# Performance work log

Measured on AMD Instinct MI355X. Metric: run time of the kernel, lower is better.

## Reference

```python
import jax, jax.numpy as jnp
import numpy as np

B, S, D, H = 4, 2048, 1024, 16
DK = D // H


def setup_inputs() -> dict:
    key = jax.random.key(0)
    ks = jax.random.split(key, 5)
    scale = 1.0 / np.sqrt(D)
    return {
        "embeddings": jax.random.normal(ks[0], (B, S, D), dtype=jnp.float32),
        "W_q": jax.random.normal(ks[1], (D, D), dtype=jnp.float32) * scale,
        "W_k": jax.random.normal(ks[2], (D, D), dtype=jnp.float32) * scale,
        "W_v": jax.random.normal(ks[3], (D, D), dtype=jnp.float32) * scale,
        "W_o": jax.random.normal(ks[4], (D, D), dtype=jnp.float32) * scale,
    }


def reference(embeddings, W_q, W_k, W_v, W_o):
    # torch Linear: y = x @ W.T  (weights stored [out, in])
    def proj(x, W):
        # [B,S,D] -> [B,H,S,DK]
        y = jnp.einsum("bsd,ed->bse", x, W)
        return y.reshape(B, S, H, DK).transpose(0, 2, 1, 3)

    Q = proj(embeddings, W_q)
    K = proj(embeddings, W_k)
    V = proj(embeddings, W_v)

    scores = jnp.einsum("bhqd,bhkd->bhqk", Q, K) / jnp.sqrt(jnp.float32(DK))
    p_attn = jax.nn.softmax(scores, axis=-1)  # dropout p=0.0 -> identity
    x = jnp.einsum("bhqk,bhkd->bhqd", p_attn, V)
    x = x.transpose(0, 2, 1, 3).reshape(B, S, D)
    return jnp.einsum("bsd,ed->bse", x, W_o)
```

## Files before the change

### kernel.cpp

```cpp
#include <hip/hip_runtime.h>
#include <hip/hip_bf16.h>

#define BB 4
#define SS 2048
#define DD 1024
#define HH 16
#define MM (BB * SS)

typedef __attribute__((ext_vector_type(8))) short bf16x8;
typedef __attribute__((ext_vector_type(4))) float f32x4;

__device__ __forceinline__ unsigned short f2bf(float f) {
  union { float f; unsigned u; } v; v.f = f;
  unsigned r = v.u + 0x7fffu + ((v.u >> 16) & 1u);
  return (unsigned short)(r >> 16);
}

__device__ __forceinline__ void gl2lds16(const void* g, void* l) {
  __builtin_amdgcn_global_load_lds(
      (const __attribute__((address_space(1))) unsigned int*)g,
      (__attribute__((address_space(3))) unsigned int*)l, 16, 0, 0);
}

__global__ __launch_bounds__(256)
void convall(const float* __restrict__ X, const float* __restrict__ a,
             const float* __restrict__ b, const float* __restrict__ c,
             const float* __restrict__ d, unsigned short* __restrict__ wall,
             unsigned short* __restrict__ xb) {
  int y = blockIdx.y;
  const float* s; unsigned short* o; float scl = 1.0f;
  if (y < 4) {
    const float* srcs[4] = {a, b, c, d};
    s = srcs[y]; o = wall + (size_t)y * 1048576;
    if (y == 0) scl = 0.180336880f;
  } else {
    s = X + (size_t)(y - 4) * 1048576; o = xb + (size_t)(y - 4) * 1048576;
  }
  int i = (blockIdx.x * 256 + threadIdx.x) * 4;
  float4 v = *(const float4*)(s + i);
  ushort4 h4;
  h4.x = f2bf(v.x * scl); h4.y = f2bf(v.y * scl);
  h4.z = f2bf(v.z * scl); h4.w = f2bf(v.w * scl);
  *(ushort4*)(o + i) = h4;
}

__global__ __launch_bounds__(512, 2)
void gemm256(const unsigned short* __restrict__ A16, const unsigned short* __restrict__ Bp,
             unsigned short* __restrict__ Qo, unsigned short* __restrict__ Ko,
             unsigned short* __restrict__ Vt) {
  extern __shared__ unsigned short L[];
  const int Lid = blockIdx.x;
  const int wg = (Lid & 7) * 48 + (Lid >> 3);
  const int mx = wg & 31, ny = wg >> 5;
  const int m0 = mx * 256, n0g = ny * 256;

  const int tid = threadIdx.x, lane = tid & 63, wv = tid >> 6;
  const int wave_m = wv >> 2, wave_n = wv & 3;
  const int row_in = lane & 15, quad = lane >> 4;

  const int srow = lane >> 3;
  const int sc = ((lane & 7) ^ (lane >> 3)) * 8;
  const unsigned short* gA0 = A16 + (size_t)(m0 + srow) * DD + sc;
  const unsigned short* gB0 = Bp + (size_t)(n0g + srow) * DD + sc;

  const int aoff = (wave_m * 128 + row_in) * 64;
  const int boff = (wave_n * 64 + row_in) * 64;
  const int swz0 = ((quad) ^ (row_in & 7)) * 8;
  const int swz1 = ((4 + quad) ^ (row_in & 7)) * 8;

  f32x4 acc[8][4] = {};

#define SA(a, par, kbv)                                                         \
  do {                                                                          \
    const int ld_ = (par) * 16384 + (a) * 8192 + (wv * 16) * 64;                \
    gl2lds16(gA0 + (size_t)((a) * 128 + wv * 16 + 0) * DD + (kbv), L + ld_);    \
    gl2lds16(gA0 + (size_t)((a) * 128 + wv * 16 + 8) * DD + (kbv), L + ld_ + 512); \
  } while (0)
#define SBf(par, kbv)                                                           \
  do {                                                                          \
    const int ld_ = 32768 + (par) * 16384 + (wv * 32) * 64;                     \
    gl2lds16(gB0 + (size_t)(wv * 32 + 0) * DD + (kbv), L + ld_);                \
    gl2lds16(gB0 + (size_t)(wv * 32 + 8) * DD + (kbv), L + ld_ + 512);          \
    gl2lds16(gB0 + (size_t)(wv * 32 + 16) * DD + (kbv), L + ld_ + 1024);        \
    gl2lds16(gB0 + (size_t)(wv * 32 + 24) * DD + (kbv), L + ld_ + 1536);        \
  } while (0)
#define LDA(par, mh, swzv)                                                      \
  do {                                                                          \
    _Pragma("unroll") for (int f = 0; f < 4; ++f)                               \
        af[f] = *(const bf16x8*)(L + (par) * 16384 + aoff + ((mh) * 64 + f * 16) * 64 + (swzv)); \
  } while (0)
#define LDB(par, swzv)                                                          \
  do {                                                                          \
    _Pragma("unroll") for (int nf = 0; nf < 4; ++nf)                            \
        bk[nf] = *(const bf16x8*)(L + 32768 + (par) * 16384 + boff + nf * 1024 + (swzv)); \
  } while (0)
#define MFMA16(mh)                                                              \
  do {                                                                          \
    __builtin_amdgcn_s_setprio(1);                                              \
    _Pragma("unroll") for (int f = 0; f < 4; ++f)                               \
        _Pragma("unroll") for (int nf = 0; nf < 4; ++nf)                        \
            acc[(mh) * 4 + f][nf] = __builtin_amdgcn_mfma_f32_16x16x32_bf16(    \
                af[f], bk[nf], acc[(mh) * 4 + f][nf], 0, 0, 0);                 \
    __builtin_amdgcn_s_setprio(0);                                              \
  } while (0)
#define PBAR()                                 \
  do {                                         \
    asm volatile("" ::: "memory");             \
    __builtin_amdgcn_s_barrier();              \
    asm volatile("" ::: "memory");             \
  } while (0)
#define PWAIT(n) asm volatile("s_waitcnt vmcnt(" #n ")" ::: "memory")

  SA(0, 0, 0);
  SBf(0, 0);
  SA(1, 0, 0);
  SA(0, 1, 64);

  for (int i = 0; i < 8; ++i) {
    const int kb1 = (2 * i + 1) * 64;
    const int t2 = 2 * i + 2, t3 = 2 * i + 3;
    const int kb2 = (t2 < 16 ? t2 : 15) * 64;
    const int kb3 = (t3 < 16 ? t3 : 15) * 64;
    bf16x8 af[4], bk[4];
    PWAIT(4); PBAR();
    LDB(0, swz0); LDA(0, 0, swz0);
    SBf(1, kb1);
    MFMA16(0);
    PWAIT(6); PBAR();
    LDA(0, 1, swz0);
    SA(1, 1, kb1);
    MFMA16(1);
    PBAR();
    LDB(0, swz1); LDA(0, 0, swz1);
    MFMA16(0);
    PBAR();
    LDA(0, 1, swz1);
    SA(0, 0, kb2);
    MFMA16(1);
    PWAIT(4); PBAR();
    LDB(1, swz0); LDA(1, 0, swz0);
    SBf(0, kb2);
    MFMA16(0);
    PWAIT(6); PBAR();
    LDA(1, 1, swz0);
    SA(1, 0, kb2);
    MFMA16(1);
    PBAR();
    LDB(1, swz1); LDA(1, 0, swz1);
    MFMA16(0);
    PBAR();
    LDA(1, 1, swz1);
    SA(0, 1, kb3);
    MFMA16(1);
  }
  asm volatile("s_waitcnt vmcnt(0)" ::: "memory");
#undef SA
#undef SBf
#undef LDA
#undef LDB
#undef MFMA16
#undef PBAR
#undef PWAIT

  const int seg = n0g >> 10;
  if (seg < 2) {
    unsigned short* Cout = (seg == 0) ? Qo : Ko;
    const int n0 = n0g & 1023;
#pragma unroll
    for (int mh = 0; mh < 2; ++mh)
#pragma unroll
      for (int f = 0; f < 4; ++f)
#pragma unroll
        for (int nf = 0; nf < 4; ++nf)
#pragma unroll
          for (int r2 = 0; r2 < 4; ++r2)
            Cout[(size_t)(m0 + wave_m * 128 + mh * 64 + f * 16 + quad * 4 + r2) * DD +
                 n0 + wave_n * 64 + nf * 16 + row_in] = f2bf(acc[mh * 4 + f][nf][r2]);
  } else {
    const int b = m0 >> 11;
    const int ktb = ((m0 & 2047) >> 6) + wave_m * 2;
    const int h = ((n0g - 2048) >> 6) + wave_n;
#pragma unroll
    for (int mh = 0; mh < 2; ++mh) {
      const int kt = ktb + mh;
#pragma unroll
      for (int nf = 0; nf < 4; ++nf) {
        unsigned short v[16];
#pragma unroll
        for (int j = 0; j < 16; ++j)
          v[j] = f2bf(acc[mh * 4 + (j & 3)][nf][j >> 2]);
        unsigned short* dst = Vt + ((size_t)((b * 16 + h) * 64 + nf * 16 + row_in)) * SS +
                              kt * 64 + quad * 16;
        *(uint4*)dst = *(const uint4*)v;
        *(uint4*)(dst + 8) = *(const uint4*)(v + 8);
      }
    }
  }
}

__global__ __launch_bounds__(256)
void gemm_o(const unsigned short* __restrict__ A16, const unsigned short* __restrict__ Bp,
            float* __restrict__ Cout) {
  __shared__ unsigned short As[2 * 4096];
  __shared__ unsigned short Bs[2 * 4096];
  const int m0 = blockIdx.x * 128, n0g = blockIdx.y * 128;
  const int tid = threadIdx.x, lane = tid & 63, wave = tid >> 6;
  const int wm = (wave & 1) * 64, wn = (wave >> 1) * 64;
  const int row_in = lane & 15, quad = lane >> 4;

  f32x4 acc[4][4] = {};

  const int r = wave * 32 + (lane >> 2);
  const unsigned short* gB = Bp + (size_t)(n0g + r) * DD + (lane & 3) * 8;
  const unsigned short* gA = A16 + (size_t)(m0 + r) * DD + (lane & 3) * 8;

  gl2lds16(gB, Bs + (wave * 32) * 32);
  gl2lds16(gB + (size_t)16 * DD, Bs + (wave * 32 + 16) * 32);
  gl2lds16(gA, As + (wave * 32) * 32);
  gl2lds16(gA + (size_t)16 * DD, As + (wave * 32 + 16) * 32);

  int cur = 0;
  for (int kb = 0; kb < DD; kb += 32) {
    __syncthreads();
    if (kb + 32 < DD) {
      const int nx = (cur ^ 1) * 4096;
      gl2lds16(gB + kb + 32, Bs + nx + (wave * 32) * 32);
      gl2lds16(gB + kb + 32 + (size_t)16 * DD, Bs + nx + (wave * 32 + 16) * 32);
      gl2lds16(gA + kb + 32, As + nx + (wave * 32) * 32);
      gl2lds16(gA + kb + 32 + (size_t)16 * DD, As + nx + (wave * 32 + 16) * 32);
    }
    const int cb = cur * 4096;
    bf16x8 af[4], bfr[4];
#pragma unroll
    for (int i = 0; i < 4; ++i)
      af[i] = *(const bf16x8*)(As + cb + (wm + i * 16 + row_in) * 32 + quad * 8);
#pragma unroll
    for (int j = 0; j < 4; ++j)
      bfr[j] = *(const bf16x8*)(Bs + cb + (wn + j * 16 + row_in) * 32 + quad * 8);
    __builtin_amdgcn_s_setprio(1);
#pragma unroll
    for (int i = 0; i < 4; ++i)
#pragma unroll
      for (int j = 0; j < 4; ++j)
        acc[i][j] = __builtin_amdgcn_mfma_f32_16x16x32_bf16(af[i], bfr[j], acc[i][j], 0, 0, 0);
    __builtin_amdgcn_s_setprio(0);
    cur ^= 1;
  }
  __syncthreads();

#pragma unroll
  for (int i = 0; i < 4; ++i)
#pragma unroll
    for (int j = 0; j < 4; ++j)
#pragma unroll
      for (int r2 = 0; r2 < 4; ++r2)
        Cout[(size_t)(m0 + wm + i * 16 + quad * 4 + r2) * DD + n0g + wn + j * 16 + row_in] =
            acc[i][j][r2];
}

__global__ __launch_bounds__(256, 4)
void attn_kernel(const unsigned short* __restrict__ Q, const unsigned short* __restrict__ K,
                 const unsigned short* __restrict__ Vt_g, unsigned short* __restrict__ AO) {
  __shared__ unsigned short Ks[64 * 72];
  __shared__ unsigned short Vs[64 * 72];
  __shared__ unsigned short Ps[128 * 72];
  const int L = (blockIdx.y << 4) + blockIdx.x;
  const int jj = L >> 3;
  const int qt = jj & 15;
  const int bh = (L & 7) + ((jj >> 4) << 3);
  const int b = bh >> 4, h = bh & 15;
  const int tid = threadIdx.x, lane = tid & 63, w = tid >> 6;
  const int row_in = lane & 15, quad = lane >> 4;
  const size_t qbase = ((size_t)(b * SS + qt * 128)) * DD + h * 64;

  bf16x8 aq[2][2];
#pragma unroll
  for (int m = 0; m < 2; ++m) {
    const unsigned short* qp = Q + qbase + (size_t)(w * 32 + m * 16 + row_in) * DD;
    aq[m][0] = *(const bf16x8*)(qp + quad * 8);
    aq[m][1] = *(const bf16x8*)(qp + 32 + quad * 8);
  }
  f32x4 oacc[2][4] = {};
  float lrow[2][4] = {};
  const int permr = 2 * (row_in >> 2) + (row_in & 1) + 8 * ((row_in >> 1) & 1);
  const int pw_base = (w * 32) * 72;

  const int r0 = tid >> 3, o80 = (tid & 7) * 8;
  const int r1 = (tid + 256) >> 3, o81 = o80;
  const unsigned short* kp0 = K + ((size_t)(b * SS + r0)) * DD + h * 64 + o80;
  const unsigned short* kp1 = K + ((size_t)(b * SS + r1)) * DD + h * 64 + o81;
  const unsigned short* vp0 = Vt_g + ((size_t)(bh * 64 + r0)) * SS + o80;
  const unsigned short* vp1 = Vt_g + ((size_t)(bh * 64 + r1)) * SS + o81;

  uint4 kr0 = *(const uint4*)kp0;
  uint4 kr1 = *(const uint4*)kp1;
  uint4 vr0 = *(const uint4*)vp0;
  uint4 vr1 = *(const uint4*)vp1;

  for (int kt = 0; kt < SS / 64; ++kt) {
    __syncthreads();
    *(uint4*)(Ks + r0 * 72 + o80) = kr0;
    *(uint4*)(Ks + r1 * 72 + o81) = kr1;
    *(uint4*)(Vs + r0 * 72 + o80) = vr0;
    *(uint4*)(Vs + r1 * 72 + o81) = vr1;
    __syncthreads();
    if (kt + 1 < SS / 64) {
      const size_t ko = (size_t)(kt + 1) * 64 * DD;
      const size_t vo = (size_t)(kt + 1) * 64;
      kr0 = *(const uint4*)(kp0 + ko);
      kr1 = *(const uint4*)(kp1 + ko);
      vr0 = *(const uint4*)(vp0 + vo);
      vr1 = *(const uint4*)(vp1 + vo);
    }

    f32x4 sacc[2][4] = {};
    __builtin_amdgcn_s_setprio(1);
#pragma unroll
    for (int n = 0; n < 4; ++n) {
      bf16x8 bk0 = *(const bf16x8*)(Ks + (n * 16 + row_in) * 72 + quad * 8);
      bf16x8 bk1 = *(const bf16x8*)(Ks + (n * 16 + row_in) * 72 + 32 + quad * 8);
#pragma unroll
      for (int m = 0; m < 2; ++m) {
        sacc[m][n] = __builtin_amdgcn_mfma_f32_16x16x32_bf16(aq[m][0], bk0, sacc[m][n], 0, 0, 0);
        sacc[m][n] = __builtin_amdgcn_mfma_f32_16x16x32_bf16(aq[m][1], bk1, sacc[m][n], 0, 0, 0);
      }
    }
    __builtin_amdgcn_s_setprio(0);

#pragma unroll
    for (int m = 0; m < 2; ++m)
#pragma unroll
      for (int r = 0; r < 4; ++r) {
        int prow = pw_base + (m * 16 + 2 * quad + (r & 1) + 8 * ((r >> 1) & 1)) * 72;
        union { float f; unsigned u; } p0, p1, p2, p3;
        p0.f = __builtin_amdgcn_exp2f(sacc[m][0][r]);
        p1.f = __builtin_amdgcn_exp2f(sacc[m][1][r]);
        p2.f = __builtin_amdgcn_exp2f(sacc[m][2][r]);
        p3.f = __builtin_amdgcn_exp2f(sacc[m][3][r]);
        lrow[m][r] += (p0.f + p1.f) + (p2.f + p3.f);
        unsigned w01 = __builtin_amdgcn_perm(p1.u + 0x8000u, p0.u + 0x8000u, 0x07060302);
        unsigned w23 = __builtin_amdgcn_perm(p3.u + 0x8000u, p2.u + 0x8000u, 0x07060302);
        *(uint2*)(Ps + prow + row_in * 4) = make_uint2(w01, w23);
      }

    __builtin_amdgcn_s_setprio(1);
#pragma unroll
    for (int c = 0; c < 2; ++c) {
      bf16x8 ap0 = *(const bf16x8*)(Ps + pw_base + (permr) * 72 + c * 32 + quad * 8);
      bf16x8 ap1 = *(const bf16x8*)(Ps + pw_base + (16 + permr) * 72 + c * 32 + quad * 8);
#pragma unroll
      for (int t = 0; t < 4; ++t) {
        bf16x8 bv = *(const bf16x8*)(Vs + (t * 16 + row_in) * 72 + c * 32 + quad * 8);
        oacc[0][t] = __builtin_amdgcn_mfma_f32_16x16x32_bf16(ap0, bv, oacc[0][t], 0, 0, 0);
        oacc[1][t] = __builtin_amdgcn_mfma_f32_16x16x32_bf16(ap1, bv, oacc[1][t], 0, 0, 0);
      }
    }
    __builtin_amdgcn_s_setprio(0);
  }

#pragma unroll
  for (int m = 0; m < 2; ++m)
#pragma unroll
    for (int r = 0; r < 4; ++r) {
#pragma unroll
      for (int s = 1; s < 16; s <<= 1) lrow[m][r] += __shfl_xor(lrow[m][r], s, 64);
      float inv = 1.0f / lrow[m][r];
#pragma unroll
      for (int t = 0; t < 4; ++t)
        AO[qbase + (size_t)(w * 32 + m * 16 + quad * 4 + r) * DD + t * 16 + row_in] =
            f2bf(oacc[m][t][r] * inv);
    }
}

extern "C" void kernel_launch(void* const* d_in, const int* in_sizes, int n_in,
                              void* d_out, int out_size, void* d_ws, size_t ws_size,
                              hipStream_t stream) {
  const float* X  = (const float*)d_in[0];
  const float* Wq = (const float*)d_in[1];
  const float* Wk = (const float*)d_in[2];
  const float* Wv = (const float*)d_in[3];
  const float* Wo = (const float*)d_in[4];

  unsigned short* ws   = (unsigned short*)d_ws;
  unsigned short* Qb   = ws;
  unsigned short* Kb   = Qb + (size_t)MM * DD;
  unsigned short* Vtb  = Kb + (size_t)MM * DD;
  unsigned short* Wall = Vtb + (size_t)MM * DD;
  unsigned short* Xb   = (unsigned short*)d_out;
  float* out = (float*)d_out;

  static int inited = 0;
  if (!inited) {
    (void)hipFuncSetAttribute((const void*)gemm256,
                              hipFuncAttributeMaxDynamicSharedMemorySize, 131072);
    inited = 1;
  }

  convall<<<dim3(1024, 12), 256, 0, stream>>>(X, Wq, Wk, Wv, Wo, Wall, Xb);

  gemm256<<<dim3(384), 512, 131072, stream>>>(Xb, Wall, Qb, Kb, Vtb);

  attn_kernel<<<dim3(SS / 128, BB * HH), 256, 0, stream>>>(Qb, Kb, Vtb, Qb);

  gemm_o<<<dim3(MM / 128, 8), 256, 0, stream>>>(Qb, Wall + (size_t)3 * 1048576, out);
}
```

Baseline: 263.6 us.

## Retile QKV GEMM to 128x256 tiles with a triple-buffered LDS pipeline

The fused QKV projection GEMM now uses 128x256 output tiles instead of 256x256, doubling the grid to 768 workgroups. The LDS loop becomes a 3-stage ring buffer that advances one 64-wide K step per iteration. Dynamic LDS grows to 144 KB to hold it. The aim is to remove the 1.5-wave tail imbalance across CUs and deepen load-compute overlap. The cost is lower arithmetic intensity per tile and more re-reads of the weight matrix.

```diff
diff --git a/kernel.cpp b/kernel.cpp
--- a/kernel.cpp
+++ b/kernel.cpp
@@ -50,9 +50,9 @@
              unsigned short* __restrict__ Vt) {
   extern __shared__ unsigned short L[];
   const int Lid = blockIdx.x;
-  const int wg = (Lid & 7) * 48 + (Lid >> 3);
-  const int mx = wg & 31, ny = wg >> 5;
-  const int m0 = mx * 256, n0g = ny * 256;
+  const int wg = (Lid & 7) * 96 + (Lid >> 3);
+  const int mx = wg & 63, ny = wg >> 6;
+  const int m0 = mx * 128, n0g = ny * 256;
 
   const int tid = threadIdx.x, lane = tid & 63, wv = tid >> 6;
   const int wave_m = wv >> 2, wave_n = wv & 3;
@@ -63,44 +63,42 @@
   const unsigned short* gA0 = A16 + (size_t)(m0 + srow) * DD + sc;
   const unsigned short* gB0 = Bp + (size_t)(n0g + srow) * DD + sc;
 
-  const int aoff = (wave_m * 128 + row_in) * 64;
+  const int aoff = (wave_m * 64 + row_in) * 64;
   const int boff = (wave_n * 64 + row_in) * 64;
   const int swz0 = ((quad) ^ (row_in & 7)) * 8;
   const int swz1 = ((4 + quad) ^ (row_in & 7)) * 8;
 
-  f32x4 acc[8][4] = {};
-
-#define SA(a, par, kbv)                                                         \
+  f32x4 acc[4][4] = {};
+
+#define SB3(p, kbv)                       \
   do {                                                                          \
-    const int ld_ = (par) * 16384 + (a) * 8192 + (wv * 16) * 64;                \
-    gl2lds16(gA0 + (size_t)((a) * 128 + wv * 16 + 0) * DD + (kbv), L + ld_);    \
-    gl2lds16(gA0 + (size_t)((a) * 128 + wv * 16 + 8) * DD + (kbv), L + ld_ + 512); \
-  } while (0)
-#define SBf(par, kbv)                                                           \
-  do {                                                                          \
-    const int ld_ = 32768 + (par) * 16384 + (wv * 32) * 64;                     \
+    const int ld_ = 24576 + (p) * 16384 + (wv * 32) * 64;                       \
     gl2lds16(gB0 + (size_t)(wv * 32 + 0) * DD + (kbv), L + ld_);                \
     gl2lds16(gB0 + (size_t)(wv * 32 + 8) * DD + (kbv), L + ld_ + 512);          \
     gl2lds16(gB0 + (size_t)(wv * 32 + 16) * DD + (kbv), L + ld_ + 1024);        \
-    gl2lds16(gB0 + (size_t)(wv * 32 + 24) * DD + (kbv), L + ld_ + 1536);        \
-  } while (0)
-#define LDA(par, mh, swzv)                                                      \
+  } while (0)
+#define SB1A(p, kbv)        \
+  do {                                                                          \
+    const int ldb_ = 24576 + (p) * 16384 + (wv * 32) * 64;                      \
+    gl2lds16(gB0 + (size_t)(wv * 32 + 24) * DD + (kbv), L + ldb_ + 1536);       \
+    const int lda_ = (p) * 8192 + (wv * 16) * 64;                               \
+    gl2lds16(gA0 + (size_t)(wv * 16 + 0) * DD + (kbv), L + lda_);               \
+    gl2lds16(gA0 + (size_t)(wv * 16 + 8) * DD + (kbv), L + lda_ + 512);         \
+  } while (0)
+#define LDAB(p, swzv)                                                           \
   do {                                                                          \
     _Pragma("unroll") for (int f = 0; f < 4; ++f)                               \
-        af[f] = *(const bf16x8*)(L + (par) * 16384 + aoff + ((mh) * 64 + f * 16) * 64 + (swzv)); \
-  } while (0)
-#define LDB(par, swzv)                                                          \
-  do {                                                                          \
+        af[f] = *(const bf16x8*)(L + (p) * 8192 + aoff + (f * 16) * 64 + (swzv)); \
     _Pragma("unroll") for (int nf = 0; nf < 4; ++nf)                            \
-        bk[nf] = *(const bf16x8*)(L + 32768 + (par) * 16384 + boff + nf * 1024 + (swzv)); \
-  } while (0)
-#define MFMA16(mh)                                                              \
+        bk[nf] = *(const bf16x8*)(L + 24576 + (p) * 16384 + boff + (nf * 16) * 64 + (swzv)); \
+  } while (0)
+#define MFMA16()                                                                \
   do {                                                                          \
     __builtin_amdgcn_s_setprio(1);                                              \
     _Pragma("unroll") for (int f = 0; f < 4; ++f)                               \
         _Pragma("unroll") for (int nf = 0; nf < 4; ++nf)                        \
-            acc[(mh) * 4 + f][nf] = __builtin_amdgcn_mfma_f32_16x16x32_bf16(    \
-                af[f], bk[nf], acc[(mh) * 4 + f][nf], 0, 0, 0);                 \
+            acc[f][nf] = __builtin_amdgcn_mfma_f32_16x16x32_bf16(               \
+                af[f], bk[nf], acc[f][nf], 0, 0, 0);                            \
     __builtin_amdgcn_s_setprio(0);                                              \
   } while (0)
 #define PBAR()                                 \
@@ -111,53 +109,28 @@
   } while (0)
 #define PWAIT(n) asm volatile("s_waitcnt vmcnt(" #n ")" ::: "memory")
 
-  SA(0, 0, 0);
-  SBf(0, 0);
-  SA(1, 0, 0);
-  SA(0, 1, 64);
-
-  for (int i = 0; i < 8; ++i) {
-    const int kb1 = (2 * i + 1) * 64;
-    const int t2 = 2 * i + 2, t3 = 2 * i + 3;
-    const int kb2 = (t2 < 16 ? t2 : 15) * 64;
-    const int kb3 = (t3 < 16 ? t3 : 15) * 64;
+  SB3(0, 0);  SB1A(0, 0);
+  SB3(1, 64); SB1A(1, 64);
+
+  int pr = 0;
+  for (int s = 0; s < 16; ++s) {
+    const int kb = (s + 2 < 16 ? s + 2 : 15) * 64;
+    const int pw = (pr == 0) ? 2 : pr - 1;
     bf16x8 af[4], bk[4];
-    PWAIT(4); PBAR();
-    LDB(0, swz0); LDA(0, 0, swz0);
-    SBf(1, kb1);
-    MFMA16(0);
     PWAIT(6); PBAR();
-    LDA(0, 1, swz0);
-    SA(1, 1, kb1);
-    MFMA16(1);
+    LDAB(pr, swz0);
+    SB3(pw, kb);
+    MFMA16();
     PBAR();
-    LDB(0, swz1); LDA(0, 0, swz1);
-    MFMA16(0);
-    PBAR();
-    LDA(0, 1, swz1);
-    SA(0, 0, kb2);
-    MFMA16(1);
-    PWAIT(4); PBAR();
-    LDB(1, swz0); LDA(1, 0, swz0);
-    SBf(0, kb2);
-    MFMA16(0);
-    PWAIT(6); PBAR();
-    LDA(1, 1, swz0);
-    SA(1, 0, kb2);
-    MFMA16(1);
-    PBAR();
-    LDB(1, swz1); LDA(1, 0, swz1);
-    MFMA16(0);
-    PBAR();
-    LDA(1, 1, swz1);
-    SA(0, 1, kb3);
-    MFMA16(1);
+    LDAB(pr, swz1);
+    SB1A(pw, kb);
+    MFMA16();
+    pr = (pr == 2) ? 0 : pr + 1;
   }
   asm volatile("s_waitcnt vmcnt(0)" ::: "memory");
-#undef SA
-#undef SBf
-#undef LDA
-#undef LDB
+#undef SB3
+#undef SB1A
+#undef LDAB
 #undef MFMA16
 #undef PBAR
 #undef PWAIT
@@ -167,33 +140,27 @@
     unsigned short* Cout = (seg == 0) ? Qo : Ko;
     const int n0 = n0g & 1023;
 #pragma unroll
-    for (int mh = 0; mh < 2; ++mh)
-#pragma unroll
-      for (int f = 0; f < 4; ++f)
-#pragma unroll
-        for (int nf = 0; nf < 4; ++nf)
-#pragma unroll
-          for (int r2 = 0; r2 < 4; ++r2)
-            Cout[(size_t)(m0 + wave_m * 128 + mh * 64 + f * 16 + quad * 4 + r2) * DD +
-                 n0 + wave_n * 64 + nf * 16 + row_in] = f2bf(acc[mh * 4 + f][nf][r2]);
+    for (int f = 0; f < 4; ++f)
+#pragma unroll
+      for (int nf = 0; nf < 4; ++nf)
+#pragma unroll
+        for (int r2 = 0; r2 < 4; ++r2)
+          Cout[(size_t)(m0 + wave_m * 64 + f * 16 + quad * 4 + r2) * DD +
+               n0 + wave_n * 64 + nf * 16 + row_in] = f2bf(acc[f][nf][r2]);
   } else {
     const int b = m0 >> 11;
-    const int ktb = ((m0 & 2047) >> 6) + wave_m * 2;
+    const int kt = ((m0 & 2047) >> 6) + wave_m;
     const int h = ((n0g - 2048) >> 6) + wave_n;
 #pragma unroll
-    for (int mh = 0; mh < 2; ++mh) {
-      const int kt = ktb + mh;
-#pragma unroll
-      for (int nf = 0; nf < 4; ++nf) {
-        unsigned short v[16];
-#pragma unroll
-        for (int j = 0; j < 16; ++j)
-          v[j] = f2bf(acc[mh * 4 + (j & 3)][nf][j >> 2]);
-        unsigned short* dst = Vt + ((size_t)((b * 16 + h) * 64 + nf * 16 + row_in)) * SS +
-                              kt * 64 + quad * 16;
-        *(uint4*)dst = *(const uint4*)v;
-        *(uint4*)(dst + 8) = *(const uint4*)(v + 8);
-      }
+    for (int nf = 0; nf < 4; ++nf) {
+      unsigned short v[16];
+#pragma unroll
+      for (int j = 0; j < 16; ++j)
+        v[j] = f2bf(acc[j & 3][nf][j >> 2]);
+      unsigned short* dst = Vt + ((size_t)((b * 16 + h) * 64 + nf * 16 + row_in)) * SS +
+                            kt * 64 + quad * 16;
+      *(uint4*)dst = *(const uint4*)v;
+      *(uint4*)(dst + 8) = *(const uint4*)(v + 8);
     }
   }
 }
@@ -392,13 +359,13 @@
   static int inited = 0;
   if (!inited) {
     (void)hipFuncSetAttribute((const void*)gemm256,
-                              hipFuncAttributeMaxDynamicSharedMemorySize, 131072);
+                              hipFuncAttributeMaxDynamicSharedMemorySize, 147456);
     inited = 1;
   }
 
   convall<<<dim3(1024, 12), 256, 0, stream>>>(X, Wq, Wk, Wv, Wo, Wall, Xb);
 
-  gemm256<<<dim3(384), 512, 131072, stream>>>(Xb, Wall, Qb, Kb, Vtb);
+  gemm256<<<dim3(768), 512, 147456, stream>>>(Xb, Wall, Qb, Kb, Vtb);
 
   attn_kernel<<<dim3(SS / 128, BB * HH), 256, 0, stream>>>(Qb, Kb, Vtb, Qb);
 
```

Measured after the change: 269.0 us. +2.0%, slower.
